# Kernel optimization log

Hardware: AMD Instinct MI355X
Metric: run time of the kernel (lower is better)

The kernel has to match this reference:

```python
import jax, jax.numpy as jnp
import numpy as np

B, D, K, H, E, Z = 64, 25000, 16, 128, 256, 32


def setup_inputs() -> dict:
    key = jax.random.key(0)
    ks = jax.random.split(key, 10)
    s = 0.02
    return {
        "x": jax.random.normal(ks[0], (B, D), jnp.float32),
        "mask": jax.random.randint(ks[1], (B, D), 0, 2, jnp.int32),
        "feat_emb": jax.random.normal(ks[2], (D, K), jnp.float32),          # feature_embedding [D,K]
        "feat_bias": jnp.zeros((D, 1), jnp.float32),                        # feature_bias [D,1]
        "W1": jax.random.normal(ks[3], (1 + K + 1, H), jnp.float32) * s,    # h_layer linear 1 (in,out)
        "b1": jnp.zeros((H,), jnp.float32),
        "W2": jax.random.normal(ks[4], (H, K), jnp.float32) * s,            # h_layer linear 2
        "b2": jnp.zeros((K,), jnp.float32),
        "We1": jax.random.normal(ks[5], (K, E), jnp.float32) * s,           # encoder_mlp linear 1
        "be1": jnp.zeros((E,), jnp.float32),
        "We2": jax.random.normal(ks[6], (E, 2 * Z), jnp.float32) * s,       # encoder_mlp linear 2
        "be2": jnp.zeros((2 * Z,), jnp.float32),
    }


def reference(x, mask, feat_emb, feat_bias, W1, b1, W2, b2, We1, be1, We2, be2):
    b, d = x.shape
    k = feat_emb.shape[1]
    # Build per-(sample, feature) input rows: [x_bd, F_d(K), bias_d] -> [B, D, 1+K+1]
    h_in = jnp.concatenate(
        [
            x[:, :, None],
            jnp.broadcast_to(feat_emb[None, :, :], (b, d, k)),
            jnp.broadcast_to(feat_bias[None, :, :], (b, d, 1)),
        ],
        axis=-1,
    )
    # Shared small MLP (h_layer), dropout is identity at rate 0.0
    h = jax.nn.relu(h_in @ W1 + b1)          # [B, D, H]
    h = jax.nn.relu(h @ W2 + b2)             # [B, D, K]
    # Masked sum pooling over features
    c = jnp.sum(h * mask.astype(h.dtype)[:, :, None], axis=1)  # [B, K]
    # encoder_mlp
    enc = jax.nn.relu(c @ We1 + be1) @ We2 + be2                # [B, 2Z]
    mu, logvar = jnp.split(enc, 2, axis=-1)
    return mu, logvar
```

## Files before the change

kernel.cpp:

```cpp
#include <hip/hip_runtime.h>
#include <hip/hip_bf16.h>

#define B 64
#define D 25000
#define K 16
#define H 128
#define E 256
#define Z 32
#define DTILE 10
#define NBLK (D / DTILE)
#define NREP 16
#define XSTR 65
#define MSTR 68

#define REP_BYTES (NREP * B * K * 4)
#define HI_OFF    REP_BYTES
#define G_OFF     (REP_BYTES + 4096)
#define WS_NEEDED (G_OFF + (size_t)D * H * 2)

typedef __attribute__((ext_vector_type(8))) _Float16 half8;
typedef __attribute__((ext_vector_type(2))) _Float16 hv2;
typedef __attribute__((ext_vector_type(4))) float f32x4;

__global__ __launch_bounds__(256) void prep_kernel(
    const float* __restrict__ W2, const float* __restrict__ feat_emb,
    const float* __restrict__ feat_bias, const float* __restrict__ W1,
    const float* __restrict__ b1, float* __restrict__ rep,
    _Float16* __restrict__ hi, _Float16* __restrict__ Gh)
{
    const int t = threadIdx.x;
    const int bid = blockIdx.x;
    if (bid < NREP) {
        for (int i = t; i < B * K; i += 256) rep[bid * B * K + i] = 0.f;
    } else if (bid == NREP) {
        for (int i = t; i < H * K; i += 256) {
            int j = i & 7, n = (i >> 3) & 15, g = (i >> 7) & 3, s = i >> 9;
            int k = s * 32 + g * 8 + j;
            hi[i] = (_Float16)W2[k * K + n];
        }
    } else {
        int idx = (bid - NREP - 1) * 256 + t;
        int d = idx >> 7, h = idx & (H - 1);
        float acc = fmaf(feat_bias[d], W1[17 * H + h], b1[h]);
        #pragma unroll
        for (int k = 0; k < K; ++k)
            acc = fmaf(feat_emb[d * K + k], W1[(1 + k) * H + h], acc);
        Gh[idx] = (_Float16)acc;
    }
}

template <bool PRE>
__global__ __launch_bounds__(256, 6) void partial_main_kernel(
    const float* __restrict__ x, const int* __restrict__ mask,
    const float* __restrict__ feat_emb, const float* __restrict__ feat_bias,
    const float* __restrict__ W1, const float* __restrict__ b1,
    const float* __restrict__ b2, const _Float16* __restrict__ Gh,
    const _Float16* __restrict__ hi, float* __restrict__ rep)
{
    __shared__ __align__(16) _Float16 sGh[DTILE * H];
    __shared__ __align__(16) float sX[DTILE * XSTR];
    __shared__ __align__(16) float sMf[DTILE * MSTR];

    const int t    = threadIdx.x;
    const int d0   = blockIdx.x * DTILE;
    const int lane = t & 63;
    const int wv   = t >> 6;
    const int g    = lane >> 4;
    const int n    = lane & 15;

    for (int i = t; i < DTILE * B; i += 256) {
        int bb = i / DTILE, dd = i - bb * DTILE;
        sX[dd * XSTR + bb]  = x[bb * D + d0 + dd];
        sMf[dd * MSTR + bb] = (float)mask[bb * D + d0 + dd];
    }
    if (PRE) {
        const unsigned* gsrc = (const unsigned*)(Gh + (size_t)d0 * H);
        unsigned* gdst = (unsigned*)sGh;
        for (int i = t; i < DTILE * H / 2; i += 256) gdst[i] = gsrc[i];
    } else {
        for (int i = t; i < DTILE * H; i += 256) {
            int dd = i >> 7, h = i & (H - 1);
            int d = d0 + dd;
            float acc = fmaf(feat_bias[d], W1[17 * H + h], b1[h]);
            #pragma unroll
            for (int k = 0; k < K; ++k)
                acc = fmaf(feat_emb[d * K + k], W1[(1 + k) * H + h], acc);
            sGh[i] = (_Float16)acc;
        }
    }

    half8 Bf[4];
    #pragma unroll
    for (int s = 0; s < 4; ++s)
        Bf[s] = *(const half8*)(hi + (((s * 4 + g) * 16 + n) << 3));
    hv2 w0h[4][4];
    #pragma unroll
    for (int s = 0; s < 4; ++s) {
        const float4* wp = (const float4*)&W1[s * 32 + g * 8];
        float4 a0 = wp[0], a1 = wp[1];
        w0h[s][0] = (hv2){(_Float16)a0.x, (_Float16)a0.y};
        w0h[s][1] = (hv2){(_Float16)a0.z, (_Float16)a0.w};
        w0h[s][2] = (hv2){(_Float16)a1.x, (_Float16)a1.y};
        w0h[s][3] = (hv2){(_Float16)a1.z, (_Float16)a1.w};
    }
    const float b2n = b2[n];
    const hv2 zeroh = {(_Float16)0.f, (_Float16)0.f};
    __syncthreads();

    f32x4 cacc = {0.f, 0.f, 0.f, 0.f};
    const int xoff = wv * 16 + n;
    const int moff = wv * 16 + g * 4;

    #pragma unroll
    for (int i = 0; i < DTILE / 2; ++i) {
        const int dd0 = 2 * i, dd1 = 2 * i + 1;
        const float xv0 = sX[dd0 * XSTR + xoff];
        const float xv1 = sX[dd1 * XSTR + xoff];
        const _Float16 xh0 = (_Float16)xv0, xh1 = (_Float16)xv1;
        const hv2 xa = {xh0, xh0}, xb = {xh1, xh1};
        f32x4 c1a = {b2n, b2n, b2n, b2n};
        f32x4 c1b = {b2n, b2n, b2n, b2n};
        #pragma unroll
        for (int s = 0; s < 4; ++s) {
            union GA { half8 v; hv2 p[4]; };
            GA ga, gb, A0, A1;
            ga.v = *(const half8*)&sGh[dd0 * H + s * 32 + g * 8];
            gb.v = *(const half8*)&sGh[dd1 * H + s * 32 + g * 8];
            #pragma unroll
            for (int p = 0; p < 4; ++p) {
                hv2 h0 = __builtin_elementwise_fma(xa, w0h[s][p], ga.p[p]);
                hv2 h1 = __builtin_elementwise_fma(xb, w0h[s][p], gb.p[p]);
                A0.p[p] = __builtin_elementwise_max(h0, zeroh);
                A1.p[p] = __builtin_elementwise_max(h1, zeroh);
            }
            c1a = __builtin_amdgcn_mfma_f32_16x16x32_f16(A0.v, Bf[s], c1a, 0, 0, 0);
            c1b = __builtin_amdgcn_mfma_f32_16x16x32_f16(A1.v, Bf[s], c1b, 0, 0, 0);
        }
        const float4 mv0 = *(const float4*)&sMf[dd0 * MSTR + moff];
        const float4 mv1 = *(const float4*)&sMf[dd1 * MSTR + moff];
        cacc[0] = fmaf(mv0.x, fmaxf(c1a[0], 0.f), fmaf(mv1.x, fmaxf(c1b[0], 0.f), cacc[0]));
        cacc[1] = fmaf(mv0.y, fmaxf(c1a[1], 0.f), fmaf(mv1.y, fmaxf(c1b[1], 0.f), cacc[1]));
        cacc[2] = fmaf(mv0.z, fmaxf(c1a[2], 0.f), fmaf(mv1.z, fmaxf(c1b[2], 0.f), cacc[2]));
        cacc[3] = fmaf(mv0.w, fmaxf(c1a[3], 0.f), fmaf(mv1.w, fmaxf(c1b[3], 0.f), cacc[3]));
    }

    float* crep = rep + (size_t)(blockIdx.x & (NREP - 1)) * (B * K);
    #pragma unroll
    for (int r = 0; r < 4; ++r)
        atomicAdd(&crep[(moff + r) * K + n], cacc[r]);
}

__global__ __launch_bounds__(256) void partial_enc_kernel(
    const float* __restrict__ rep, const float* __restrict__ We1,
    const float* __restrict__ be1, const float* __restrict__ We2,
    const float* __restrict__ be2, float* __restrict__ out)
{
    const int b = blockIdx.x;
    const int t = threadIdx.x;
    __shared__ float sc[K];
    __shared__ float st1[E];
    __shared__ float red[256];

    {
        const int k = t & 15, grp = t >> 4;
        red[t] = rep[grp * (B * K) + b * K + k];
    }
    __syncthreads();
    if (t < K) {
        float s2 = 0.f;
        #pragma unroll
        for (int q = 0; q < 16; ++q) s2 += red[q * 16 + t];
        sc[t] = s2;
    }
    __syncthreads();

    {
        float acc = be1[t];
        #pragma unroll
        for (int k = 0; k < K; ++k)
            acc = fmaf(sc[k], We1[k * E + t], acc);
        st1[t] = fmaxf(acc, 0.f);
    }
    __syncthreads();

    const int j = t & 63, seg = t >> 6;
    float acc = 0.f;
    #pragma unroll 4
    for (int e = seg * 64; e < seg * 64 + 64; ++e)
        acc = fmaf(st1[e], We2[e * 64 + j], acc);
    red[t] = acc;
    __syncthreads();

    if (t < 64) {
        float v = red[j] + red[64 + j] + red[128 + j] + red[192 + j] + be2[j];
        if (j < Z) out[b * Z + j] = v;
        else       out[B * Z + b * Z + (j - Z)] = v;
    }
}

extern "C" void kernel_launch(void* const* d_in, const int* in_sizes, int n_in,
                              void* d_out, int out_size, void* d_ws, size_t ws_size,
                              hipStream_t stream) {
    const float* x         = (const float*)d_in[0];
    const int*   mask      = (const int*)  d_in[1];
    const float* feat_emb  = (const float*)d_in[2];
    const float* feat_bias = (const float*)d_in[3];
    const float* W1        = (const float*)d_in[4];
    const float* b1        = (const float*)d_in[5];
    const float* W2        = (const float*)d_in[6];
    const float* b2        = (const float*)d_in[7];
    const float* We1       = (const float*)d_in[8];
    const float* be1       = (const float*)d_in[9];
    const float* We2       = (const float*)d_in[10];
    const float* be2       = (const float*)d_in[11];

    float*     rep = (float*)d_ws;
    _Float16*  hi  = (_Float16*)((char*)d_ws + HI_OFF);
    _Float16*  Gh  = (_Float16*)((char*)d_ws + G_OFF);

    const bool big = (ws_size >= WS_NEEDED);
    const int  gblocks = big ? (D * H / 256) : 0;

    prep_kernel<<<NREP + 1 + gblocks, 256, 0, stream>>>(
        W2, feat_emb, feat_bias, W1, b1, rep, hi, Gh);
    if (big)
        partial_main_kernel<true><<<NBLK, 256, 0, stream>>>(
            x, mask, feat_emb, feat_bias, W1, b1, b2, Gh, hi, rep);
    else
        partial_main_kernel<false><<<NBLK, 256, 0, stream>>>(
            x, mask, feat_emb, feat_bias, W1, b1, b2, Gh, hi, rep);
    partial_enc_kernel<<<B, 256, 0, stream>>>(
        rep, We1, be1, We2, be2, (float*)d_out);
}
```

Measured before the change: 122.7 us.

## Read x and precomputed G directly from global memory, bypassing LDS staging

Each lane now loads its x values straight from global memory into registers as half pairs, and in the precomputed path reads G rows directly from global instead of copying them into shared memory first. The x shared-memory tile is removed and the occupancy hint on the launch bounds is dropped. The aim is to cut LDS staging traffic and shared-memory footprint. In exchange, global reads of G are repeated by every wave (relying on cache), the float2 loads of x assume 8-byte alignment that odd tile offsets may not guarantee, and register allocation may change without the occupancy hint.

```diff
diff --git a/kernel.cpp b/kernel.cpp
--- a/kernel.cpp
+++ b/kernel.cpp
@@ -10,7 +10,6 @@
 #define DTILE 10
 #define NBLK (D / DTILE)
 #define NREP 16
-#define XSTR 65
 #define MSTR 68
 
 #define REP_BYTES (NREP * B * K * 4)
@@ -50,16 +49,15 @@
 }
 
 template <bool PRE>
-__global__ __launch_bounds__(256, 6) void partial_main_kernel(
+__global__ __launch_bounds__(256) void partial_main_kernel(
     const float* __restrict__ x, const int* __restrict__ mask,
     const float* __restrict__ feat_emb, const float* __restrict__ feat_bias,
     const float* __restrict__ W1, const float* __restrict__ b1,
     const float* __restrict__ b2, const _Float16* __restrict__ Gh,
     const _Float16* __restrict__ hi, float* __restrict__ rep)
 {
+    __shared__ __align__(16) float sMf[DTILE * MSTR];
     __shared__ __align__(16) _Float16 sGh[DTILE * H];
-    __shared__ __align__(16) float sX[DTILE * XSTR];
-    __shared__ __align__(16) float sMf[DTILE * MSTR];
 
     const int t    = threadIdx.x;
     const int d0   = blockIdx.x * DTILE;
@@ -70,14 +68,9 @@
 
     for (int i = t; i < DTILE * B; i += 256) {
         int bb = i / DTILE, dd = i - bb * DTILE;
-        sX[dd * XSTR + bb]  = x[bb * D + d0 + dd];
         sMf[dd * MSTR + bb] = (float)mask[bb * D + d0 + dd];
     }
-    if (PRE) {
-        const unsigned* gsrc = (const unsigned*)(Gh + (size_t)d0 * H);
-        unsigned* gdst = (unsigned*)sGh;
-        for (int i = t; i < DTILE * H / 2; i += 256) gdst[i] = gsrc[i];
-    } else {
+    if (!PRE) {
         for (int i = t; i < DTILE * H; i += 256) {
             int dd = i >> 7, h = i & (H - 1);
             int d = d0 + dd;
@@ -89,6 +82,14 @@
         }
     }
 
+    const float* xrow = x + (size_t)(wv * 16 + n) * D + d0;
+    hv2 xh[DTILE / 2];
+    #pragma unroll
+    for (int i = 0; i < DTILE / 2; ++i) {
+        float2 xv = *(const float2*)(xrow + 2 * i);
+        xh[i] = (hv2){(_Float16)xv.x, (_Float16)xv.y};
+    }
+
     half8 Bf[4];
     #pragma unroll
     for (int s = 0; s < 4; ++s)
@@ -105,27 +106,28 @@
     }
     const float b2n = b2[n];
     const hv2 zeroh = {(_Float16)0.f, (_Float16)0.f};
+
+    const _Float16* gb0;
+    if (PRE) gb0 = Gh + (size_t)d0 * H + g * 8;
+    else     gb0 = sGh + g * 8;
     __syncthreads();
 
     f32x4 cacc = {0.f, 0.f, 0.f, 0.f};
-    const int xoff = wv * 16 + n;
     const int moff = wv * 16 + g * 4;
 
     #pragma unroll
     for (int i = 0; i < DTILE / 2; ++i) {
         const int dd0 = 2 * i, dd1 = 2 * i + 1;
-        const float xv0 = sX[dd0 * XSTR + xoff];
-        const float xv1 = sX[dd1 * XSTR + xoff];
-        const _Float16 xh0 = (_Float16)xv0, xh1 = (_Float16)xv1;
-        const hv2 xa = {xh0, xh0}, xb = {xh1, xh1};
+        const hv2 xa = {xh[i].x, xh[i].x};
+        const hv2 xb = {xh[i].y, xh[i].y};
         f32x4 c1a = {b2n, b2n, b2n, b2n};
         f32x4 c1b = {b2n, b2n, b2n, b2n};
         #pragma unroll
         for (int s = 0; s < 4; ++s) {
             union GA { half8 v; hv2 p[4]; };
             GA ga, gb, A0, A1;
-            ga.v = *(const half8*)&sGh[dd0 * H + s * 32 + g * 8];
-            gb.v = *(const half8*)&sGh[dd1 * H + s * 32 + g * 8];
+            ga.v = *(const half8*)(gb0 + dd0 * H + s * 32);
+            gb.v = *(const half8*)(gb0 + dd1 * H + s * 32);
             #pragma unroll
             for (int p = 0; p < 4; ++p) {
                 hv2 h0 = __builtin_elementwise_fma(xa, w0h[s][p], ga.p[p]);
```

New measurement: 124.0 us. About the same (+1.1%).
